# Kernel tuning notes

Hardware: AMD Instinct MI355X
Metric: run time of the kernel (lower is better)

The kernel has to match this reference:

```python
import jax, jax.numpy as jnp
import numpy as np

S, B, D, H, HD = 2048, 4, 1280, 16, 80  # seq, batch, d_model, heads, head_dim
NSEG = 8


def setup_inputs() -> dict:
    key = jax.random.key(0)
    k0, k1, k2 = jax.random.split(key, 3)
    x = jax.random.normal(k0, (S, B, D), dtype=jnp.float32)
    Wqkv = jax.random.normal(k1, (D, 3 * D), dtype=jnp.float32) * 0.02
    bqkv = jnp.zeros((3 * D,), dtype=jnp.float32)
    Wproj = jax.random.normal(k2, (D, 4 * D), dtype=jnp.float32) * 0.02
    bproj = jnp.zeros((4 * D,), dtype=jnp.float32)
    # 8 equal windows of 256 tokens: [0, 256, 512, ..., 2048]
    cu_seqlens = (jnp.arange(NSEG + 1, dtype=jnp.int32) * (S // NSEG))
    return {"x": x, "Wqkv": Wqkv, "bqkv": bqkv, "Wproj": Wproj,
            "bproj": bproj, "cu_seqlens": cu_seqlens}


def reference(x, Wqkv, bqkv, Wproj, bproj, cu_seqlens):
    s, b, d = x.shape
    qkv = x @ Wqkv + bqkv                     # [s, b, 3d]
    q, k, v = jnp.split(qkv, 3, axis=2)       # each [s, b, d]
    def to_bhsd(t):
        return t.reshape(s, b, H, HD).transpose(1, 2, 0, 3)  # [b, h, s, hd]
    q, k, v = to_bhsd(q), to_bhsd(k), to_bhsd(v)
    # Block-diagonal mask: token t belongs to window searchsorted(cu[1:], t, right)
    pos = jnp.arange(s)
    seg = jnp.searchsorted(cu_seqlens[1:], pos, side='right')  # [s]
    bias = jnp.where(seg[:, None] == seg[None, :], 0.0,
                     jnp.finfo(x.dtype).min)                   # [s, s]
    scale = 1.0 / jnp.sqrt(jnp.asarray(HD, dtype=x.dtype))
    scores = jnp.einsum('bhsd,bhtd->bhst', q, k) * scale + bias
    attn = jax.nn.softmax(scores, axis=-1)
    out = jnp.einsum('bhst,bhtd->bhsd', attn, v)               # [b, h, s, hd]
    context = out.transpose(2, 0, 1, 3).reshape(s, b, H * HD)  # [s, b, d]
    return context @ Wproj + bproj                             # [s, b, 4d]
```

## Files before the change

### kernel.cpp

```cpp
#include <hip/hip_runtime.h>

typedef _Float16 f16;
typedef _Float16 f16x8 __attribute__((ext_vector_type(8)));
typedef _Float16 f16x4 __attribute__((ext_vector_type(4)));
typedef float    f32x4 __attribute__((ext_vector_type(4)));
typedef unsigned int u32t;

#define AS1 __attribute__((address_space(1)))
#define AS3 __attribute__((address_space(3)))

static __device__ __forceinline__ void gload_lds16(const void* g, void* l) {
  __builtin_amdgcn_global_load_lds((const AS1 u32t*)g, (AS3 u32t*)l, 16, 0, 0);
}

static __device__ __forceinline__ f16x8 zero8() {
  f16x8 z;
#pragma unroll
  for (int j = 0; j < 8; ++j) z[j] = (f16)0;
  return z;
}

__global__ void k_cvt_x(const float* __restrict__ in, f16* __restrict__ out, int n4) {
  int stride = gridDim.x * blockDim.x;
  for (int i = blockIdx.x * blockDim.x + threadIdx.x; i < n4; i += stride) {
    float4 v = ((const float4*)in)[i];
    f16x4 o;
    o[0] = (f16)v.x; o[1] = (f16)v.y; o[2] = (f16)v.z; o[3] = (f16)v.w;
    ((f16x4*)out)[i] = o;
  }
}

__global__ void k_cvt_w_t(const float* __restrict__ W, f16* __restrict__ Wt, int N) {
  __shared__ float T[32][33];
  int bk = blockIdx.x % 40;
  int bn = blockIdx.x / 40;
  int k0 = bk * 32, n0 = bn * 32;
  int r = threadIdx.x >> 5;
  int c = threadIdx.x & 31;
#pragma unroll
  for (int i = 0; i < 4; ++i)
    T[r + i * 8][c] = W[(size_t)(k0 + r + i * 8) * N + n0 + c];
  __syncthreads();
#pragma unroll
  for (int i = 0; i < 4; ++i)
    Wt[(size_t)(n0 + r + i * 8) * 1280 + k0 + c] = (f16)T[c][r + i * 8];
}

template<int NCOLS, bool F16OUT>
__global__ __launch_bounds__(256, 2)
void gemm_nt(const f16* __restrict__ A, const f16* __restrict__ Bt,
             const float* __restrict__ bias, void* __restrict__ Cout)
{
  __shared__ __align__(16) f16 sA[128 * 64];
  __shared__ __align__(16) f16 sB[128 * 64];
  const int tid = threadIdx.x;
  const int wave = tid >> 6, lane = tid & 63;
  constexpr int NBN = NCOLS / 128;
  const int bm = blockIdx.x / NBN, bn = blockIdx.x % NBN;
  const long row0 = (long)bm * 128, col0 = (long)bn * 128;

  f32x4 acc[4][4];
#pragma unroll
  for (int i = 0; i < 4; ++i)
#pragma unroll
    for (int j = 0; j < 4; ++j) acc[i][j] = (f32x4){0.f, 0.f, 0.f, 0.f};

  const int wr = (wave >> 1) * 64, wc = (wave & 1) * 64;

  int segr[4], segoff[4];
#pragma unroll
  for (int i = 0; i < 4; ++i) {
    int o = (wave * 4 + i) * 1024 + lane * 16;
    int r = o >> 7, cb = o & 127;
    segr[i] = r;
    segoff[i] = cb ^ ((r & 7) << 4);
  }

  const char* Ab = (const char*)A;
  const char* Bb = (const char*)Bt;

  for (int kt = 0; kt < 20; ++kt) {
    __syncthreads();
#pragma unroll
    for (int i = 0; i < 4; ++i) {
      const char* ga = Ab + ((row0 + segr[i]) * 1280 + kt * 64) * 2 + segoff[i];
      gload_lds16(ga, (char*)sA + (wave * 4 + i) * 1024);
      const char* gb = Bb + ((col0 + segr[i]) * 1280 + kt * 64) * 2 + segoff[i];
      gload_lds16(gb, (char*)sB + (wave * 4 + i) * 1024);
    }
    __syncthreads();

#pragma unroll
    for (int kk = 0; kk < 2; ++kk) {
      const int rl = lane & 15, g = lane >> 4, x7 = lane & 7;
      const int ph = (kk * 4 + g) ^ x7;
      f16x8 af[4], bf[4];
#pragma unroll
      for (int mt = 0; mt < 4; ++mt)
        af[mt] = *(const f16x8*)(sA + (wr + mt * 16 + rl) * 64 + ph * 8);
#pragma unroll
      for (int nt = 0; nt < 4; ++nt)
        bf[nt] = *(const f16x8*)(sB + (wc + nt * 16 + rl) * 64 + ph * 8);
#pragma unroll
      for (int mt = 0; mt < 4; ++mt)
#pragma unroll
        for (int nt = 0; nt < 4; ++nt)
          acc[mt][nt] = __builtin_amdgcn_mfma_f32_16x16x32_f16(af[mt], bf[nt], acc[mt][nt], 0, 0, 0);
    }
  }

  const int rl = lane & 15, g = lane >> 4;
#pragma unroll
  for (int mt = 0; mt < 4; ++mt) {
#pragma unroll
    for (int nt = 0; nt < 4; ++nt) {
      long c = col0 + wc + nt * 16 + rl;
      float bv = bias[c];
#pragma unroll
      for (int r = 0; r < 4; ++r) {
        long rr = row0 + wr + mt * 16 + g * 4 + r;
        float v = acc[mt][nt][r] + bv;
        if (F16OUT) ((f16*)Cout)[rr * NCOLS + c] = (f16)v;
        else        ((float*)Cout)[rr * NCOLS + c] = v;
      }
    }
  }
}

__global__ void k_vt(const f16* __restrict__ qkv, f16* __restrict__ vt) {
  __shared__ __align__(16) f16 T[128 * 136];
  int bid = blockIdx.x;
  int sc16 = bid & 15, bh = bid >> 4;
  int b = bh >> 4, h = bh & 15;
  int s0 = sc16 * 128;
  int t = threadIdx.x;
#pragma unroll
  for (int i = 0; i < 5; ++i) {
    int cid = i * 256 + t;
    int s = cid / 10, c = cid % 10;
    const f16* g = qkv + (size_t)((s0 + s) * 4 + b) * 3840 + 2560 + h * 80 + c * 8;
    f16x8 v = *(const f16x8*)g;
    int phys = c ^ ((s >> 3) & 7);
    *(f16x8*)(T + s * 136 + phys * 8) = v;
  }
  __syncthreads();
#pragma unroll
  for (int i = 0; i < 5; ++i) {
    int oid = i * 256 + t;
    int sc8 = oid & 15, hd = oid >> 4;
    f16x8 o;
#pragma unroll
    for (int j = 0; j < 8; ++j) {
      int row = sc8 * 8 + j;
      int phys = (hd >> 3) ^ (sc8 & 7);
      o[j] = T[row * 136 + phys * 8 + (hd & 7)];
    }
    *(f16x8*)(vt + (size_t)(bh * 80 + hd) * 2048 + s0 + sc8 * 8) = o;
  }
}

__global__ __launch_bounds__(512, 2)
void k_attn(const f16* __restrict__ qkv, const f16* __restrict__ vt,
            f16* __restrict__ ctx)
{
  __shared__ __align__(16) f16 sK[256 * 104];
  __shared__ __align__(16) f16 sV[80 * 264];
  __shared__ __align__(16) f16 sP[128 * 72];

  const int bid = blockIdx.x;
  const int qc = bid & 1, seg = (bid >> 1) & 7, h = (bid >> 4) & 15, b = bid >> 8;
  const int t = threadIdx.x;
  const int wave = t >> 6, lane = t & 63;
  const int s_key0 = seg * 256;

#pragma unroll
  for (int i = 0; i < 5; ++i) {
    int cid = i * 512 + t;
    int key = cid / 10, c = cid % 10;
    const f16* g = qkv + (size_t)((s_key0 + key) * 4 + b) * 3840 + 1280 + h * 80 + c * 8;
    *(f16x8*)(sK + key * 104 + c * 8) = *(const f16x8*)g;
  }
  {
    int key = t >> 1, c = t & 1;
    *(f16x8*)(sK + key * 104 + 80 + c * 8) = zero8();
  }
#pragma unroll
  for (int i = 0; i < 5; ++i) {
    int cid = i * 512 + t;
    int hd = cid >> 5, c = cid & 31;
    const f16* g = vt + (size_t)((b * 16 + h) * 80 + hd) * 2048 + s_key0 + c * 8;
    *(f16x8*)(sV + hd * 264 + c * 8) = *(const f16x8*)g;
  }

  const int q0 = s_key0 + qc * 128 + wave * 16;
  const int rl = lane & 15, g = lane >> 4;
  f16x8 qf[3];
  {
    const f16* gq = qkv + (size_t)((q0 + rl) * 4 + b) * 3840 + h * 80;
    qf[0] = *(const f16x8*)(gq + g * 8);
    qf[1] = *(const f16x8*)(gq + 32 + g * 8);
    if (g < 2) qf[2] = *(const f16x8*)(gq + 64 + g * 8);
    else       qf[2] = zero8();
  }
  __syncthreads();

  f32x4 sc[16];
#pragma unroll
  for (int nt = 0; nt < 16; ++nt) sc[nt] = (f32x4){0.f, 0.f, 0.f, 0.f};
#pragma unroll
  for (int nt = 0; nt < 16; ++nt) {
#pragma unroll
    for (int kk = 0; kk < 3; ++kk) {
      f16x8 bf = *(const f16x8*)(sK + (nt * 16 + rl) * 104 + kk * 32 + g * 8);
      sc[nt] = __builtin_amdgcn_mfma_f32_16x16x32_f16(qf[kk], bf, sc[nt], 0, 0, 0);
    }
  }

  const float scale = 0.11180339887498949f;
  float inv[4];
#pragma unroll
  for (int r = 0; r < 4; ++r) {
    float m = -1e30f;
#pragma unroll
    for (int nt = 0; nt < 16; ++nt) m = fmaxf(m, sc[nt][r]);
#pragma unroll
    for (int off = 8; off >= 1; off >>= 1) m = fmaxf(m, __shfl_xor(m, off));
    m *= scale;
    float sum = 0.f;
#pragma unroll
    for (int nt = 0; nt < 16; ++nt) {
      float p = __expf(sc[nt][r] * scale - m);
      sc[nt][r] = p;
      sum += p;
    }
#pragma unroll
    for (int off = 8; off >= 1; off >>= 1) sum += __shfl_xor(sum, off);
    inv[r] = 1.0f / sum;
  }

  f32x4 o[5];
#pragma unroll
  for (int nt = 0; nt < 5; ++nt) o[nt] = (f32x4){0.f, 0.f, 0.f, 0.f};
  const int prow0 = wave * 16;
  for (int ch = 0; ch < 4; ++ch) {
    __syncthreads();
#pragma unroll
    for (int f = 0; f < 4; ++f) {
      int nt = ch * 4 + f;
#pragma unroll
      for (int r = 0; r < 4; ++r)
        sP[(prow0 + g * 4 + r) * 72 + f * 16 + rl] = (f16)sc[nt][r];
    }
    __syncthreads();
#pragma unroll
    for (int kk = 0; kk < 2; ++kk) {
      f16x8 pa = *(const f16x8*)(sP + (prow0 + rl) * 72 + kk * 32 + g * 8);
#pragma unroll
      for (int nt = 0; nt < 5; ++nt) {
        f16x8 vb = *(const f16x8*)(sV + (nt * 16 + rl) * 264 + ch * 64 + kk * 32 + g * 8);
        o[nt] = __builtin_amdgcn_mfma_f32_16x16x32_f16(pa, vb, o[nt], 0, 0, 0);
      }
    }
  }

#pragma unroll
  for (int nt = 0; nt < 5; ++nt) {
    int hd = nt * 16 + rl;
#pragma unroll
    for (int r = 0; r < 4; ++r) {
      long qrow = q0 + g * 4 + r;
      float v = o[nt][r] * inv[r];
      ctx[(qrow * 4 + b) * 1280 + h * 80 + hd] = (f16)v;
    }
  }
}

extern "C" void kernel_launch(void* const* d_in, const int* in_sizes, int n_in,
                              void* d_out, int out_size, void* d_ws, size_t ws_size,
                              hipStream_t stream)
{
  const float* x     = (const float*)d_in[0];
  const float* Wqkv  = (const float*)d_in[1];
  const float* bqkv  = (const float*)d_in[2];
  const float* Wproj = (const float*)d_in[3];
  const float* bproj = (const float*)d_in[4];

  char* ws = (char*)d_ws;
  f16* X16   = (f16*)(ws);
  f16* WQT   = (f16*)(ws + 20971520);
  f16* WPT   = (f16*)(ws + 30801920);
  f16* QKV16 = (f16*)(ws + 43909120);
  f16* VT    = (f16*)(ws + 106823680);
  f16* CTX16 = X16;

  k_cvt_x<<<4096, 256, 0, stream>>>(x, X16, 8192 * 1280 / 4);
  k_cvt_w_t<<<40 * 120, 256, 0, stream>>>(Wqkv, WQT, 3840);
  k_cvt_w_t<<<40 * 160, 256, 0, stream>>>(Wproj, WPT, 5120);
  gemm_nt<3840, true ><<<64 * 30, 256, 0, stream>>>(X16, WQT, bqkv, QKV16);
  k_vt<<<1024, 256, 0, stream>>>(QKV16, VT);
  k_attn<<<1024, 512, 0, stream>>>(QKV16, VT, CTX16);
  gemm_nt<5120, false><<<64 * 40, 256, 0, stream>>>(CTX16, WPT, bproj, d_out);
}
```

Measured before the change: 285.8 us.

## Rewrite GEMM as 256x256-tile, 4-stage LDS-pipelined kernel with XCD-aware block mapping

The fp16 NT GEMM used for the QKV and output projections moves from 128x128 tiles with one LDS buffer and two barriers per k-step to 256x256 tiles on 512 threads. It uses a 4-deep ring of direct global-to-LDS loads, so loads for tile t+3 are issued while MFMAs run on tile t, synchronised by vmcnt waits and one barrier per tile. It also raises MFMA priority with s_setprio and remaps block IDs so neighbouring tiles land on the same XCD. The aim is to hide global load latency and raise operand reuse. In exchange it uses 128 KB of LDS, which limits occupancy to one block per CU, and the LDS reads are unswizzled, which may cause bank conflicts.

```diff
diff --git a/kernel.cpp b/kernel.cpp
--- a/kernel.cpp
+++ b/kernel.cpp
@@ -46,80 +46,133 @@
     Wt[(size_t)(n0 + r + i * 8) * 1280 + k0 + c] = (f16)T[c][r + i * 8];
 }
 
+
+template<int VM, bool STAGE>
+static __device__ __forceinline__ void ktile(
+    int t, int ts_buf,
+    const char* const (&gA)[2], const char* const (&gB)[2],
+    char* const (&dA)[2], char* const (&dB)[2],
+    char* bA, char* bB,
+    const int (&offA)[8], const int (&offB)[4], f32x4 (&acc)[8][4])
+{
+  if constexpr (STAGE) {
+    const long ko = (long)(t + 3) * 64;
+#pragma unroll
+    for (int l = 0; l < 2; ++l) gload_lds16(gA[l] + ko, dA[l] + ts_buf * 16384);
+  }
+  f16x8 af[8];
+#pragma unroll
+  for (int f = 0; f < 8; ++f) af[f] = *(const f16x8*)(bA + offA[f]);
+  f16x8 b0 = *(const f16x8*)(bB + offB[0]);
+  f16x8 b1 = *(const f16x8*)(bB + offB[1]);
+  __builtin_amdgcn_s_setprio(1);
+#pragma unroll
+  for (int f = 0; f < 8; ++f)
+    acc[f][0] = __builtin_amdgcn_mfma_f32_16x16x32_f16(af[f], b0, acc[f][0], 0, 0, 0);
+#pragma unroll
+  for (int f = 0; f < 8; ++f)
+    acc[f][1] = __builtin_amdgcn_mfma_f32_16x16x32_f16(af[f], b1, acc[f][1], 0, 0, 0);
+  __builtin_amdgcn_s_setprio(0);
+  if constexpr (STAGE) {
+    const long ko = (long)(t + 3) * 64;
+#pragma unroll
+    for (int l = 0; l < 2; ++l) gload_lds16(gB[l] + ko, dB[l] + ts_buf * 16384);
+  }
+  f16x8 b2 = *(const f16x8*)(bB + offB[2]);
+  f16x8 b3 = *(const f16x8*)(bB + offB[3]);
+  __builtin_amdgcn_s_setprio(1);
+#pragma unroll
+  for (int f = 0; f < 8; ++f)
+    acc[f][2] = __builtin_amdgcn_mfma_f32_16x16x32_f16(af[f], b2, acc[f][2], 0, 0, 0);
+#pragma unroll
+  for (int f = 0; f < 8; ++f)
+    acc[f][3] = __builtin_amdgcn_mfma_f32_16x16x32_f16(af[f], b3, acc[f][3], 0, 0, 0);
+  __builtin_amdgcn_s_setprio(0);
+  if constexpr (VM >= 0) {
+    asm volatile("s_waitcnt vmcnt(%0)" :: "n"(VM) : "memory");
+    __builtin_amdgcn_s_barrier();
+    asm volatile("" ::: "memory");
+  }
+}
+
 template<int NCOLS, bool F16OUT>
-__global__ __launch_bounds__(256, 2)
+__global__ __launch_bounds__(512, 2)
 void gemm_nt(const f16* __restrict__ A, const f16* __restrict__ Bt,
              const float* __restrict__ bias, void* __restrict__ Cout)
 {
-  __shared__ __align__(16) f16 sA[128 * 64];
-  __shared__ __align__(16) f16 sB[128 * 64];
+  __shared__ __align__(16) char lds[131072];
+  char* ldsA = lds;
+  char* ldsB = lds + 65536;
+
   const int tid = threadIdx.x;
   const int wave = tid >> 6, lane = tid & 63;
-  constexpr int NBN = NCOLS / 128;
-  const int bm = blockIdx.x / NBN, bn = blockIdx.x % NBN;
-  const long row0 = (long)bm * 128, col0 = (long)bn * 128;
-
-  f32x4 acc[4][4];
-#pragma unroll
-  for (int i = 0; i < 4; ++i)
-#pragma unroll
-    for (int j = 0; j < 4; ++j) acc[i][j] = (f32x4){0.f, 0.f, 0.f, 0.f};
-
-  const int wr = (wave >> 1) * 64, wc = (wave & 1) * 64;
-
-  int segr[4], segoff[4];
-#pragma unroll
-  for (int i = 0; i < 4; ++i) {
-    int o = (wave * 4 + i) * 1024 + lane * 16;
-    int r = o >> 7, cb = o & 127;
-    segr[i] = r;
-    segoff[i] = cb ^ ((r & 7) << 4);
-  }
-
-  const char* Ab = (const char*)A;
-  const char* Bb = (const char*)Bt;
-
-  for (int kt = 0; kt < 20; ++kt) {
-    __syncthreads();
-#pragma unroll
-    for (int i = 0; i < 4; ++i) {
-      const char* ga = Ab + ((row0 + segr[i]) * 1280 + kt * 64) * 2 + segoff[i];
-      gload_lds16(ga, (char*)sA + (wave * 4 + i) * 1024);
-      const char* gb = Bb + ((col0 + segr[i]) * 1280 + kt * 64) * 2 + segoff[i];
-      gload_lds16(gb, (char*)sB + (wave * 4 + i) * 1024);
-    }
-    __syncthreads();
-
-#pragma unroll
-    for (int kk = 0; kk < 2; ++kk) {
-      const int rl = lane & 15, g = lane >> 4, x7 = lane & 7;
-      const int ph = (kk * 4 + g) ^ x7;
-      f16x8 af[4], bf[4];
-#pragma unroll
-      for (int mt = 0; mt < 4; ++mt)
-        af[mt] = *(const f16x8*)(sA + (wr + mt * 16 + rl) * 64 + ph * 8);
-#pragma unroll
-      for (int nt = 0; nt < 4; ++nt)
-        bf[nt] = *(const f16x8*)(sB + (wc + nt * 16 + rl) * 64 + ph * 8);
-#pragma unroll
-      for (int mt = 0; mt < 4; ++mt)
-#pragma unroll
-        for (int nt = 0; nt < 4; ++nt)
-          acc[mt][nt] = __builtin_amdgcn_mfma_f32_16x16x32_f16(af[mt], bf[nt], acc[mt][nt], 0, 0, 0);
-    }
-  }
-
   const int rl = lane & 15, g = lane >> 4;
-#pragma unroll
-  for (int mt = 0; mt < 4; ++mt) {
-#pragma unroll
-    for (int nt = 0; nt < 4; ++nt) {
-      long c = col0 + wc + nt * 16 + rl;
+  const int wm = wave >> 2, wn = wave & 3;
+
+  constexpr int NBN = NCOLS / 256;
+  constexpr int NWG = 32 * NBN;
+  const int bid = blockIdx.x;
+  const int wgid = (bid & 7) * (NWG / 8) + (bid >> 3);
+  const int bm = wgid / NBN, bn = wgid % NBN;
+  const long row0 = (long)bm * 256, col0 = (long)bn * 256;
+
+  const char* gA[2]; const char* gB[2]; char* dA[2]; char* dB[2];
+#pragma unroll
+  for (int l = 0; l < 2; ++l) {
+    int seg = wave * 2 + l;
+    int p = seg * 1024 + lane * 16;
+    int row = p >> 6, colB = p & 63;
+    gA[l] = (const char*)A  + (row0 + row) * 2560 + colB;
+    gB[l] = (const char*)Bt + (col0 + row) * 2560 + colB;
+    dA[l] = ldsA + seg * 1024;
+    dB[l] = ldsB + seg * 1024;
+  }
+
+  int offA[8], offB[4];
+#pragma unroll
+  for (int f = 0; f < 8; ++f) offA[f] = (wm * 128 + f * 16 + rl) * 64 + g * 16;
+#pragma unroll
+  for (int n = 0; n < 4; ++n) offB[n] = (wn * 64 + n * 16 + rl) * 64 + g * 16;
+
+  f32x4 acc[8][4];
+#pragma unroll
+  for (int f = 0; f < 8; ++f)
+#pragma unroll
+    for (int n = 0; n < 4; ++n) acc[f][n] = (f32x4){0.f, 0.f, 0.f, 0.f};
+
+#pragma unroll
+  for (int t = 0; t < 3; ++t) {
+#pragma unroll
+    for (int l = 0; l < 2; ++l) gload_lds16(gA[l] + t * 64, dA[l] + t * 16384);
+#pragma unroll
+    for (int l = 0; l < 2; ++l) gload_lds16(gB[l] + t * 64, dB[l] + t * 16384);
+  }
+  asm volatile("s_waitcnt vmcnt(8)" ::: "memory");
+  __builtin_amdgcn_s_barrier();
+  asm volatile("" ::: "memory");
+
+  for (int tt = 0; tt < 9; ++tt) {
+    const int t = tt * 4;
+    ktile<8, true>(t + 0, 3, gA, gB, dA, dB, ldsA + 0 * 16384, ldsB + 0 * 16384, offA, offB, acc);
+    ktile<8, true>(t + 1, 0, gA, gB, dA, dB, ldsA + 1 * 16384, ldsB + 1 * 16384, offA, offB, acc);
+    ktile<8, true>(t + 2, 1, gA, gB, dA, dB, ldsA + 2 * 16384, ldsB + 2 * 16384, offA, offB, acc);
+    ktile<8, true>(t + 3, 2, gA, gB, dA, dB, ldsA + 3 * 16384, ldsB + 3 * 16384, offA, offB, acc);
+  }
+  ktile<8, true >(36, 3, gA, gB, dA, dB, ldsA + 0 * 16384, ldsB + 0 * 16384, offA, offB, acc);
+  ktile<4, false>(37, 0, gA, gB, dA, dB, ldsA + 1 * 16384, ldsB + 1 * 16384, offA, offB, acc);
+  ktile<0, false>(38, 0, gA, gB, dA, dB, ldsA + 2 * 16384, ldsB + 2 * 16384, offA, offB, acc);
+  ktile<-1, false>(39, 0, gA, gB, dA, dB, ldsA + 3 * 16384, ldsB + 3 * 16384, offA, offB, acc);
+
+#pragma unroll
+  for (int f = 0; f < 8; ++f) {
+#pragma unroll
+    for (int n = 0; n < 4; ++n) {
+      long c = col0 + wn * 64 + n * 16 + rl;
       float bv = bias[c];
 #pragma unroll
       for (int r = 0; r < 4; ++r) {
-        long rr = row0 + wr + mt * 16 + g * 4 + r;
-        float v = acc[mt][nt][r] + bv;
+        long rr = row0 + wm * 128 + f * 16 + g * 4 + r;
+        float v = acc[f][n][r] + bv;
         if (F16OUT) ((f16*)Cout)[rr * NCOLS + c] = (f16)v;
         else        ((float*)Cout)[rr * NCOLS + c] = v;
       }
@@ -296,8 +349,8 @@
   k_cvt_x<<<4096, 256, 0, stream>>>(x, X16, 8192 * 1280 / 4);
   k_cvt_w_t<<<40 * 120, 256, 0, stream>>>(Wqkv, WQT, 3840);
   k_cvt_w_t<<<40 * 160, 256, 0, stream>>>(Wproj, WPT, 5120);
-  gemm_nt<3840, true ><<<64 * 30, 256, 0, stream>>>(X16, WQT, bqkv, QKV16);
+  gemm_nt<3840, true ><<<480, 512, 0, stream>>>(X16, WQT, bqkv, QKV16);
   k_vt<<<1024, 256, 0, stream>>>(QKV16, VT);
   k_attn<<<1024, 512, 0, stream>>>(QKV16, VT, CTX16);
-  gemm_nt<5120, false><<<64 * 40, 256, 0, stream>>>(CTX16, WPT, bproj, d_out);
-}
+  gemm_nt<5120, false><<<640, 512, 0, stream>>>(CTX16, WPT, bproj, d_out);
+}
```

Result: slower. 295.2 us (+3.3%).

## Rewrite GEMM as 256x256 tile, 8-wave, double-buffered pipelined kernel

Applied to the files above, without the earlier changes.

Replaces the 128x128 single-buffered GEMM with a 256x256 tile computed by 512 threads (8 waves) and a 128 KB double-buffered LDS. Global-to-LDS loads for the next K slice are interleaved between MFMA quarter-blocks using raw barriers, vmcnt waits and s_setprio, so memory traffic overlaps compute. A block-ID remap groups workgroups for L2 locality. In exchange it uses a large LDS footprint and much heavier register pressure, and the hand-written wait/barrier schedule is fragile.

```diff
diff --git a/kernel.cpp b/kernel.cpp
--- a/kernel.cpp
+++ b/kernel.cpp
@@ -46,80 +46,148 @@
     Wt[(size_t)(n0 + r + i * 8) * 1280 + k0 + c] = (f16)T[c][r + i * 8];
 }
 
+
 template<int NCOLS, bool F16OUT>
-__global__ __launch_bounds__(256, 2)
+__global__ __launch_bounds__(512, 2)
 void gemm_nt(const f16* __restrict__ A, const f16* __restrict__ Bt,
              const float* __restrict__ bias, void* __restrict__ Cout)
 {
-  __shared__ __align__(16) f16 sA[128 * 64];
-  __shared__ __align__(16) f16 sB[128 * 64];
+  __shared__ __align__(16) char lds[131072];
   const int tid = threadIdx.x;
   const int wave = tid >> 6, lane = tid & 63;
-  constexpr int NBN = NCOLS / 128;
-  const int bm = blockIdx.x / NBN, bn = blockIdx.x % NBN;
-  const long row0 = (long)bm * 128, col0 = (long)bn * 128;
-
-  f32x4 acc[4][4];
-#pragma unroll
-  for (int i = 0; i < 4; ++i)
-#pragma unroll
-    for (int j = 0; j < 4; ++j) acc[i][j] = (f32x4){0.f, 0.f, 0.f, 0.f};
-
-  const int wr = (wave >> 1) * 64, wc = (wave & 1) * 64;
-
-  int segr[4], segoff[4];
-#pragma unroll
-  for (int i = 0; i < 4; ++i) {
-    int o = (wave * 4 + i) * 1024 + lane * 16;
-    int r = o >> 7, cb = o & 127;
-    segr[i] = r;
-    segoff[i] = cb ^ ((r & 7) << 4);
-  }
-
-  const char* Ab = (const char*)A;
-  const char* Bb = (const char*)Bt;
-
-  for (int kt = 0; kt < 20; ++kt) {
-    __syncthreads();
-#pragma unroll
-    for (int i = 0; i < 4; ++i) {
-      const char* ga = Ab + ((row0 + segr[i]) * 1280 + kt * 64) * 2 + segoff[i];
-      gload_lds16(ga, (char*)sA + (wave * 4 + i) * 1024);
-      const char* gb = Bb + ((col0 + segr[i]) * 1280 + kt * 64) * 2 + segoff[i];
-      gload_lds16(gb, (char*)sB + (wave * 4 + i) * 1024);
-    }
-    __syncthreads();
-
-#pragma unroll
-    for (int kk = 0; kk < 2; ++kk) {
-      const int rl = lane & 15, g = lane >> 4, x7 = lane & 7;
-      const int ph = (kk * 4 + g) ^ x7;
-      f16x8 af[4], bf[4];
-#pragma unroll
-      for (int mt = 0; mt < 4; ++mt)
-        af[mt] = *(const f16x8*)(sA + (wr + mt * 16 + rl) * 64 + ph * 8);
-#pragma unroll
-      for (int nt = 0; nt < 4; ++nt)
-        bf[nt] = *(const f16x8*)(sB + (wc + nt * 16 + rl) * 64 + ph * 8);
-#pragma unroll
-      for (int mt = 0; mt < 4; ++mt)
-#pragma unroll
-        for (int nt = 0; nt < 4; ++nt)
-          acc[mt][nt] = __builtin_amdgcn_mfma_f32_16x16x32_f16(af[mt], bf[nt], acc[mt][nt], 0, 0, 0);
-    }
-  }
-
   const int rl = lane & 15, g = lane >> 4;
-#pragma unroll
-  for (int mt = 0; mt < 4; ++mt) {
-#pragma unroll
-    for (int nt = 0; nt < 4; ++nt) {
-      long c = col0 + wc + nt * 16 + rl;
+  const int wm = wave >> 2, wn = wave & 3;
+
+  constexpr int NBN = NCOLS / 256;
+  constexpr int NWG = 32 * NBN;
+  const int bid = blockIdx.x;
+  const int wgid = (bid & 7) * (NWG / 8) + (bid >> 3);
+  const int bm = wgid / NBN, bn = wgid % NBN;
+  const long row0 = (long)bm * 256, col0 = (long)bn * 256;
+
+  const int srow = tid >> 3;
+  const int scol = ((tid & 7) ^ (srow & 7)) << 4;
+  const char* gA = (const char*)A  + (row0 + srow) * 2560 + scol;
+  const char* gB = (const char*)Bt + (col0 + srow) * 2560 + scol;
+  char* const ldsw = lds + wave * 1024;
+
+  auto STAGE = [&](int isB, int buf, int half, int kb) {
+    const char* s = (isB ? gB : gA) + half * (128 * 2560) + kb;
+    char* d = ldsw + isB * 65536 + buf * 32768 + half * 16384;
+    gload_lds16(s, d);
+    gload_lds16(s + 64 * 2560, d + 8192);
+  };
+
+  const int swz0 = ((0 + g) ^ (rl & 7)) << 4;
+  const int swz1 = ((4 + g) ^ (rl & 7)) << 4;
+  const int aoff = (wm * 128 + rl) << 7;
+  const int boff = 65536 + ((wn * 64 + rl) << 7);
+
+  auto LDA = [&](f16x8 (&af)[8], int buf, int mh) {
+#pragma unroll
+    for (int m = 0; m < 4; ++m) {
+      const char* p = lds + buf * 32768 + aoff + (mh * 4 + m) * 2048;
+      af[m * 2 + 0] = *(const f16x8*)(p + swz0);
+      af[m * 2 + 1] = *(const f16x8*)(p + swz1);
+    }
+  };
+  auto LDB = [&](f16x8 (&bf)[4], int buf, int nh) {
+#pragma unroll
+    for (int n = 0; n < 2; ++n) {
+      const char* p = lds + buf * 32768 + boff + (nh * 2 + n) * 2048;
+      bf[n * 2 + 0] = *(const f16x8*)(p + swz0);
+      bf[n * 2 + 1] = *(const f16x8*)(p + swz1);
+    }
+  };
+
+  f32x4 acc[8][4];
+#pragma unroll
+  for (int m = 0; m < 8; ++m)
+#pragma unroll
+    for (int n = 0; n < 4; ++n) acc[m][n] = (f32x4){0.f, 0.f, 0.f, 0.f};
+
+  auto MM = [&](int mh, int nh, const f16x8 (&af)[8], const f16x8 (&bf)[4]) {
+    __builtin_amdgcn_s_setprio(1);
+#pragma unroll
+    for (int m = 0; m < 4; ++m)
+#pragma unroll
+      for (int n = 0; n < 2; ++n)
+#pragma unroll
+        for (int kk = 0; kk < 2; ++kk)
+          acc[mh * 4 + m][nh * 2 + n] = __builtin_amdgcn_mfma_f32_16x16x32_f16(
+              af[m * 2 + kk], bf[n * 2 + kk], acc[mh * 4 + m][nh * 2 + n], 0, 0, 0);
+    __builtin_amdgcn_s_setprio(0);
+  };
+
+#define BAR()    __builtin_amdgcn_s_barrier()
+#define WLGKM()  asm volatile("s_waitcnt lgkmcnt(0)" ::: "memory")
+#define WVM(N)   asm volatile("s_waitcnt vmcnt(" #N ")" ::: "memory")
+
+  auto TILE = [&](int buf,
+                  int s0b, int s0u, int s0h, int s0k,
+                  int s1b, int s1u, int s1h, int s1k,
+                  int s2b, int s2u, int s2h, int s2k,
+                  int s3b, int s3u, int s3h, int s3k,
+                  int vmend, bool endbar) {
+    f16x8 af[8], bf0[4], bf1[4];
+    LDA(af, buf, 0); LDB(bf0, buf, 0);
+    if (s0k >= 0) STAGE(s0b, s0u, s0h, s0k);
+    BAR(); WLGKM(); MM(0, 0, af, bf0); BAR();
+    LDB(bf1, buf, 1);
+    if (s1k >= 0) STAGE(s1b, s1u, s1h, s1k);
+    BAR(); WLGKM(); MM(0, 1, af, bf1); BAR();
+    LDA(af, buf, 1);
+    if (s2k >= 0) STAGE(s2b, s2u, s2h, s2k);
+    BAR(); WLGKM(); MM(1, 1, af, bf1); BAR();
+    if (s3k >= 0) STAGE(s3b, s3u, s3h, s3k);
+    BAR(); MM(1, 0, af, bf0);
+    if (vmend == 2) WVM(2);
+    else if (vmend == 0) WVM(0);
+    if (endbar) BAR();
+  };
+
+  STAGE(0, 0, 0, 0); STAGE(0, 0, 1, 0); STAGE(1, 0, 0, 0); STAGE(1, 0, 1, 0);
+  STAGE(0, 1, 0, 128);
+  WVM(2); BAR();
+
+#pragma unroll 1
+  for (int it = 0; it < 9; ++it) {
+    const int kb = it * 256;
+    TILE(0,
+         0, 1, 1, kb + 128,
+         1, 1, 0, kb + 128,
+         1, 1, 1, kb + 128,
+         0, 0, 0, kb + 256,
+         2, true);
+    TILE(1,
+         0, 0, 1, kb + 256,
+         1, 0, 0, kb + 256,
+         1, 0, 1, kb + 256,
+         0, 1, 0, kb + 384,
+         2, true);
+  }
+  TILE(0,
+       0, 1, 1, 2432,
+       1, 1, 0, 2432,
+       1, 1, 1, 2432,
+       0, 0, 0, -1,
+       0, true);
+  TILE(1, 0,0,0,-1, 0,0,0,-1, 0,0,0,-1, 0,0,0,-1, -1, false);
+
+#undef BAR
+#undef WLGKM
+#undef WVM
+
+#pragma unroll
+  for (int m = 0; m < 8; ++m) {
+#pragma unroll
+    for (int n = 0; n < 4; ++n) {
+      long c = col0 + wn * 64 + n * 16 + rl;
       float bv = bias[c];
 #pragma unroll
       for (int r = 0; r < 4; ++r) {
-        long rr = row0 + wr + mt * 16 + g * 4 + r;
-        float v = acc[mt][nt][r] + bv;
+        long rr = row0 + wm * 128 + m * 16 + g * 4 + r;
+        float v = acc[m][n][r] + bv;
         if (F16OUT) ((f16*)Cout)[rr * NCOLS + c] = (f16)v;
         else        ((float*)Cout)[rr * NCOLS + c] = v;
       }
@@ -296,8 +364,8 @@
   k_cvt_x<<<4096, 256, 0, stream>>>(x, X16, 8192 * 1280 / 4);
   k_cvt_w_t<<<40 * 120, 256, 0, stream>>>(Wqkv, WQT, 3840);
   k_cvt_w_t<<<40 * 160, 256, 0, stream>>>(Wproj, WPT, 5120);
-  gemm_nt<3840, true ><<<64 * 30, 256, 0, stream>>>(X16, WQT, bqkv, QKV16);
+  gemm_nt<3840, true ><<<480, 512, 0, stream>>>(X16, WQT, bqkv, QKV16);
   k_vt<<<1024, 256, 0, stream>>>(QKV16, VT);
   k_attn<<<1024, 512, 0, stream>>>(QKV16, VT, CTX16);
-  gemm_nt<5120, false><<<64 * 40, 256, 0, stream>>>(CTX16, WPT, bproj, d_out);
-}
+  gemm_nt<5120, false><<<640, 512, 0, stream>>>(CTX16, WPT, bproj, d_out);
+}
```

Result: no change. 281.5 us (-1.5%).
